# Optimization experiments

Measured on AMD Instinct MI355X. Metric: run time of the kernel, lower is better.

Reference implementation:

```python
import jax, jax.numpy as jnp
import numpy as np

ADMP = 8  # admp_channel -> K = ADMP*ADMP keypoints


def setup_inputs() -> dict:
    key = jax.random.key(0)
    kA, kB = jax.random.split(key)
    B, C, H, W = 8, 512, 96, 96
    feature_A = jax.random.normal(kA, (B, C, H, W), dtype=jnp.float32)
    feature_B = jax.random.normal(kB, (B, C, H, W), dtype=jnp.float32)
    return {"feature_A": feature_A, "feature_B": feature_B}


def _keypoint_rowcol(feature_A):
    # featureSelect: sum over channels, AdaptiveMaxPool2d(ADMP) with return_indices.
    # H,W divisible by ADMP so adaptive pool == uniform non-overlapping pooling.
    B, C, H, W = feature_A.shape
    ph, pw = H // ADMP, W // ADMP
    resp = feature_A.sum(axis=1)  # [B,H,W]
    r = resp.reshape(B, ADMP, ph, ADMP, pw).transpose(0, 1, 3, 2, 4)
    r = r.reshape(B, ADMP * ADMP, ph * pw)
    loc = jnp.argmax(r, axis=-1)  # first-max, matches torch  [B,K]
    kk = jnp.arange(ADMP * ADMP)
    gi, gj = kk // ADMP, kk % ADMP
    row_A = gi[None, :] * ph + loc // pw  # [B,K]
    col_A = gj[None, :] * pw + loc % pw
    return row_A, col_A


def reference(feature_A, feature_B):
    B, C, H, W = feature_A.shape
    K = ADMP * ADMP
    row_A, col_A = _keypoint_rowcol(feature_A)
    flat_A = row_A * W + col_A  # [B,K]

    # gather descriptors: [B,K,C]
    fa = feature_A.reshape(B, C, H * W)
    desc = jnp.take_along_axis(fa, flat_A[:, None, :], axis=2).transpose(0, 2, 1)

    # squared L2 distance map via ||b||^2 - 2 a.b + ||a||^2 : [B,K,HW]
    fb = feature_B.reshape(B, C, H * W)
    fb_sq = jnp.sum(fb * fb, axis=1)            # [B,HW]
    d_sq = jnp.sum(desc * desc, axis=-1)        # [B,K]
    cross = jnp.einsum('bkc,bcn->bkn', desc, fb)  # [B,K,HW]
    dist = fb_sq[:, None, :] - 2.0 * cross + d_sq[:, :, None]

    min_idx = jnp.argmin(dist, axis=-1)  # [B,K]
    row_B = min_idx // W
    col_B = min_idx % W
    drow = -(row_B - row_A)
    dcol = -(col_B - col_A)
    off = jnp.stack([drow, dcol], axis=-1)  # [B,K,2] int

    # getTranslationalOffsetByMode: most frequent (drow,dcol) pair per batch
    eq = jnp.all(off[:, :, None, :] == off[:, None, :, :], axis=-1)  # [B,K,K]
    counts = eq.sum(axis=-1)  # [B,K]
    best = jnp.argmax(counts, axis=-1)  # first occurrence on ties, matches dict order
    out = jnp.take_along_axis(off, best[:, None, None], axis=1)[:, 0, :]  # [B,2]
    return out
```

## Files before the change

kernel.cpp:

```cpp
#include <hip/hip_runtime.h>
#include <hip/hip_bf16.h>
#include <math.h>

typedef _Float16 half8 __attribute__((ext_vector_type(8)));
typedef __fp16 fp16x2 __attribute__((ext_vector_type(2)));
typedef float f32x4 __attribute__((ext_vector_type(4)));
typedef unsigned short u16x4 __attribute__((ext_vector_type(4)));
typedef unsigned short u16x8 __attribute__((ext_vector_type(8)));

#define B_   8
#define C_   512
#define H_   96
#define W_   96
#define HW   9216
#define K_   64
#define PH   12
#define PW   12
#define NT   96
#define CCH  32
#define NBLK 96

#define OFF_PARTIAL 0u
#define OFF_CANDV   0u
#define OFF_CANDN   294912u
#define OFF_DESCH   2359296u
#define OFF_DESCL   2883584u
#define OFF_ROWA    3407872u
#define OFF_COLA    3409920u

#define FBT_HI 0
#define FBT_LO 3072
#define DSC_HI 6144
#define DSC_LO 8704
#define BUFHW  11264

__global__ __launch_bounds__(256) void k_partial(const float* __restrict__ A,
                                                 float* __restrict__ part) {
    int idx4 = blockIdx.x * 256 + threadIdx.x;
    int chunk = blockIdx.y;
    int b = idx4 / (HW / 4), hw4 = idx4 - b * (HW / 4);
    const float* p = A + ((size_t)(b * C_ + chunk * 64)) * HW + hw4 * 4;
    float4 s = make_float4(0.f, 0.f, 0.f, 0.f);
#pragma unroll
    for (int i = 0; i < 64; ++i) {
        float4 v = *(const float4*)&p[(size_t)i * HW];
        s.x += v.x; s.y += v.y; s.z += v.z; s.w += v.w;
    }
    *(float4*)&part[chunk * (B_ * HW) + b * HW + hw4 * 4] = s;
}

__global__ void k_selgather(const float* __restrict__ part, const float* __restrict__ A,
                            int* __restrict__ rowA, int* __restrict__ colA,
                            _Float16* __restrict__ descH, _Float16* __restrict__ descL) {
    int k = blockIdx.x, b = blockIdx.y, lane = threadIdx.x;
    int gi = k >> 3, gj = k & 7;
    float bv = -1e30f; int bp = 1 << 20;
    for (int p = lane; p < PH * PW; p += 64) {
        int lr = p / PW, lc = p - lr * PW;
        int hw = (gi * PH + lr) * W_ + gj * PW + lc;
        float v = 0.f;
#pragma unroll
        for (int ch = 0; ch < 8; ++ch) v += part[ch * (B_ * HW) + b * HW + hw];
        if (v > bv || (v == bv && p < bp)) { bv = v; bp = p; }
    }
    for (int m = 1; m < 64; m <<= 1) {
        float ov = __shfl_xor(bv, m);
        int   op = __shfl_xor(bp, m);
        if (ov > bv || (ov == bv && op < bp)) { bv = ov; bp = op; }
    }
    int lr = bp / PW, lc = bp - lr * PW;
    int r = gi * PH + lr, c = gj * PW + lc;
    int flat = r * W_ + c;
    if (lane == 0) { rowA[b * K_ + k] = r; colA[b * K_ + k] = c; }
#pragma unroll
    for (int i = 0; i < 8; ++i) {
        int cc = i * 64 + lane;
        float v = A[((size_t)(b * C_ + cc)) * HW + flat];
        _Float16 h = (_Float16)v;
        _Float16 lo = (_Float16)((v - (float)h) * 2048.f);
        size_t o = ((size_t)(b * K_ + k)) * C_ + cc;
        descH[o] = h; descL[o] = lo;
    }
}

__global__ __launch_bounds__(256, 3) void k_main(const float* __restrict__ FB,
                                                 const _Float16* __restrict__ descH,
                                                 const _Float16* __restrict__ descL,
                                                 float* __restrict__ candV,
                                                 int* __restrict__ candN) {
    __shared__ __attribute__((aligned(16))) unsigned short smem_us[2 * BUFHW];
    int b = blockIdx.y, nb = blockIdx.x * NT;
    int tid = threadIdx.x;
    int l = tid & 63;
    int w = tid >> 6;
    const size_t baseB = (size_t)b * C_ * HW + nb;

    const int so = tid % 12;
    const int scb = tid / 12;
    const int st_nt = so >> 1, st_nn0 = (so & 1) * 8;
    const int dk = tid >> 2, dco = tid & 3;

    f32x4 accH[6], accX[6];
#pragma unroll
    for (int nt = 0; nt < 6; ++nt) {
        accH[nt] = (f32x4){0.f, 0.f, 0.f, 0.f};
        accX[nt] = (f32x4){0.f, 0.f, 0.f, 0.f};
    }
    float sq[8];
#pragma unroll
    for (int j = 0; j < 8; ++j) sq[j] = 0.f;

    float4 Ar0a, Ar0b, Ar1a, Ar1b; u16x8 ArdH, ArdL;
    float4 Br0a, Br0b, Br1a, Br1b; u16x8 BrdH, BrdL;

#define LOADALL(S, c0)                                                        \
    do {                                                                      \
        if (tid < 192) {                                                      \
            const float* p0 = &FB[baseB + (size_t)((c0) + scb) * HW + so * 8];      \
            const float* p1 = &FB[baseB + (size_t)((c0) + scb + 16) * HW + so * 8]; \
            S##r0a = *(const float4*)p0; S##r0b = *(const float4*)(p0 + 4);   \
            S##r1a = *(const float4*)p1; S##r1b = *(const float4*)(p1 + 4);   \
        }                                                                     \
        size_t o = ((size_t)(b * K_) + dk) * C_ + (c0) + dco * 8;             \
        S##rdH = *(const u16x8*)&descH[o];                                    \
        S##rdL = *(const u16x8*)&descL[o];                                    \
    } while (0)

#define CVT8(va, vb, hofs)                                                    \
    do {                                                                      \
        union { fp16x2 p[4]; half8 h; } hh, ll;                               \
        float vv[8] = {va.x, va.y, va.z, va.w, vb.x, vb.y, vb.z, vb.w};       \
        _Pragma("unroll")                                                     \
        for (int j = 0; j < 4; ++j) {                                         \
            float a = vv[2 * j], bq = vv[2 * j + 1];                          \
            fp16x2 hp = __builtin_amdgcn_cvt_pkrtz(a, bq);                    \
            float ha = (float)hp[0], hb = (float)hp[1];                       \
            fp16x2 lp = __builtin_amdgcn_cvt_pkrtz((a - ha) * 2048.f,         \
                                                   (bq - hb) * 2048.f);       \
            hh.p[j] = hp; ll.p[j] = lp;                                       \
            sq[2 * j]     = fmaf(a, a, sq[2 * j]);                            \
            sq[2 * j + 1] = fmaf(bq, bq, sq[2 * j + 1]);                      \
        }                                                                     \
        *(half8*)&smem_us[(hofs)] = hh.h;                                     \
        *(half8*)&smem_us[(hofs) + FBT_LO] = ll.h;                            \
    } while (0)

#define WRITEALL(S, bufhw)                                                    \
    do {                                                                      \
        if (tid < 192) {                                                      \
            int c = scb;                                                      \
            int off0 = (bufhw) + FBT_HI + st_nt * 512 + ((c >> 2) & 1) * 256  \
                       + (c >> 3) * 64 + (c & 3) * 16 + st_nn0;               \
            CVT8(S##r0a, S##r0b, off0);                                       \
            c = scb + 16;                                                     \
            int off1 = (bufhw) + FBT_HI + st_nt * 512 + ((c >> 2) & 1) * 256  \
                       + (c >> 3) * 64 + (c & 3) * 16 + st_nn0;               \
            CVT8(S##r1a, S##r1b, off1);                                       \
        }                                                                     \
        *(u16x8*)&smem_us[(bufhw) + DSC_HI + dk * 40 + dco * 8] = S##rdH;     \
        *(u16x8*)&smem_us[(bufhw) + DSC_LO + dk * 40 + dco * 8] = S##rdL;     \
    } while (0)

    const unsigned lds0 = (unsigned)(size_t)&smem_us[0];

#define TRQ(d0, d1, d2, d3, addr)                                             \
    asm volatile("ds_read_b64_tr_b16 %0, %1"             : "=v"(d0) : "v"(addr)); \
    asm volatile("ds_read_b64_tr_b16 %0, %1 offset:512"  : "=v"(d1) : "v"(addr)); \
    asm volatile("ds_read_b64_tr_b16 %0, %1 offset:6144" : "=v"(d2) : "v"(addr)); \
    asm volatile("ds_read_b64_tr_b16 %0, %1 offset:6656" : "=v"(d3) : "v"(addr));

#define WAIT8 asm volatile("s_waitcnt lgkmcnt(8)" ::: "memory");              \
              __builtin_amdgcn_sched_barrier(0);
#define WAIT4 asm volatile("s_waitcnt lgkmcnt(4)" ::: "memory");              \
              __builtin_amdgcn_sched_barrier(0);
#define WAIT0 asm volatile("s_waitcnt lgkmcnt(0)" ::: "memory");              \
              __builtin_amdgcn_sched_barrier(0);

#define MFMA3(nt, h0_, h1_, l0_, l1_)                                         \
    do {                                                                      \
        union { u16x4 q[2]; half8 h; } bh, bl;                                \
        bh.q[0] = h0_; bh.q[1] = h1_; bl.q[0] = l0_; bl.q[1] = l1_;           \
        accH[nt] = __builtin_amdgcn_mfma_f32_16x16x32_f16(aHu.h, bh.h, accH[nt], 0, 0, 0); \
        accX[nt] = __builtin_amdgcn_mfma_f32_16x16x32_f16(aHu.h, bl.h, accX[nt], 0, 0, 0); \
        accX[nt] = __builtin_amdgcn_mfma_f32_16x16x32_f16(aLu.h, bh.h, accX[nt], 0, 0, 0); \
    } while (0)

#define COMPUTE(cur)                                                          \
    do {                                                                      \
        union { u16x8 u; half8 h; } aHu, aLu;                                 \
        const unsigned abase = lds0 +                                         \
            (unsigned)((cur) + DSC_HI + (w * 16 + (l & 15)) * 40 + (l >> 4) * 8) * 2u; \
        __builtin_amdgcn_s_setprio(1);                                        \
        asm volatile("ds_read_b128 %0, %1"             : "=v"(aHu.u) : "v"(abase)); \
        asm volatile("ds_read_b128 %0, %1 offset:5120" : "=v"(aLu.u) : "v"(abase)); \
        const unsigned trb = lds0 + (unsigned)(cur) * 2u + (unsigned)l * 8u;  \
        u16x4 xh0, xh1, xl0, xl1, yh0, yh1, yl0, yl1, zh0, zh1, zl0, zl1;     \
        TRQ(xh0, xh1, xl0, xl1, trb);                                 \
        TRQ(yh0, yh1, yl0, yl1, trb + 1024u);                         \
        TRQ(zh0, zh1, zl0, zl1, trb + 2048u);                         \
        WAIT8;                                              \
        MFMA3(0, xh0, xh1, xl0, xl1);                                         \
        TRQ(xh0, xh1, xl0, xl1, trb + 3072u);                         \
        WAIT8;                                                  \
        MFMA3(1, yh0, yh1, yl0, yl1);                                         \
        TRQ(yh0, yh1, yl0, yl1, trb + 4096u);                         \
        WAIT8;                                                  \
        MFMA3(2, zh0, zh1, zl0, zl1);                                         \
        TRQ(zh0, zh1, zl0, zl1, trb + 5120u);                         \
        WAIT8;                                                  \
        MFMA3(3, xh0, xh1, xl0, xl1);                                         \
        WAIT4;                                                  \
        MFMA3(4, yh0, yh1, yl0, yl1);                                         \
        WAIT0;                                                  \
        MFMA3(5, zh0, zh1, zl0, zl1);                                         \
        __builtin_amdgcn_s_setprio(0);                                        \
    } while (0)

    LOADALL(A, 0);
    WRITEALL(A, 0);
    LOADALL(B, CCH);
    __syncthreads();

#pragma unroll 1
    for (int tp = 0; tp < 8; ++tp) {
        const int t0 = 2 * tp, t1 = 2 * tp + 1;
        if (t0 + 2 < 16) LOADALL(A, (t0 + 2) * CCH);
        COMPUTE(0);
        if (t0 + 1 < 16) WRITEALL(B, BUFHW);
        __syncthreads();
        if (t1 + 2 < 16) LOADALL(B, (t1 + 2) * CCH);
        COMPUTE(BUFHW);
        if (t1 + 1 < 16) WRITEALL(A, 0);
        __syncthreads();
    }

    float* fscr = (float*)&smem_us[0];
    if (tid < 192) {
        *(float4*)&fscr[scb * 96 + so * 8]     = make_float4(sq[0], sq[1], sq[2], sq[3]);
        *(float4*)&fscr[scb * 96 + so * 8 + 4] = make_float4(sq[4], sq[5], sq[6], sq[7]);
    }
    __syncthreads();
    if (tid < 96) {
        float s = 0.f;
#pragma unroll
        for (int g = 0; g < 16; ++g) s += fscr[g * 96 + tid];
        fscr[1536 + tid] = s;
    }
    __syncthreads();

    const float inv2048 = 1.f / 2048.f;
#pragma unroll
    for (int r = 0; r < 4; ++r) {
        float bv = 1e30f; int bn = 1 << 28;
#pragma unroll
        for (int nt = 0; nt < 6; ++nt) {
            float cross = accH[nt][r] + accX[nt][r] * inv2048;
            float d = fscr[1536 + nt * 16 + (l & 15)] - 2.f * cross;
            int n = nb + nt * 16 + (l & 15);
            if (d < bv) { bv = d; bn = n; }
        }
#pragma unroll
        for (int m = 1; m < 16; m <<= 1) {
            float ov = __shfl_xor(bv, m);
            int   on = __shfl_xor(bn, m);
            if (ov < bv || (ov == bv && on < bn)) { bv = ov; bn = on; }
        }
        if ((l & 15) == 0) {
            int k = w * 16 + (l >> 4) * 4 + r;
            candV[(b * K_ + k) * NBLK + blockIdx.x] = bv;
            candN[(b * K_ + k) * NBLK + blockIdx.x] = bn;
        }
    }
#undef LOADALL
#undef CVT8
#undef WRITEALL
#undef TRQ
#undef WAIT8
#undef WAIT4
#undef WAIT0
#undef MFMA3
#undef COMPUTE
}

__global__ void k_redmode(const float* __restrict__ candV, const int* __restrict__ candN,
                          const int* __restrict__ rowA, const int* __restrict__ colA,
                          int* __restrict__ out) {
    __shared__ int r_s[64], c_s[64];
    int b = blockIdx.x, k = threadIdx.x;
    int base = (b * K_ + k) * NBLK;
    float bv = 1e30f; int bn = 1 << 28;
    for (int j = 0; j < NBLK; ++j) {
        float ov = candV[base + j]; int on = candN[base + j];
        if (ov < bv || (ov == bv && on < bn)) { bv = ov; bn = on; }
    }
    int rB = bn / W_, cB = bn - rB * W_;
    r_s[k] = rowA[b * K_ + k] - rB;
    c_s[k] = colA[b * K_ + k] - cB;
    __syncthreads();
    int mr = r_s[k], mc = c_s[k], cnt = 0;
#pragma unroll
    for (int j = 0; j < 64; ++j) cnt += (r_s[j] == mr && c_s[j] == mc) ? 1 : 0;
    int bk = k, bc = cnt;
    for (int m = 1; m < 64; m <<= 1) {
        int oc = __shfl_xor(bc, m);
        int ok = __shfl_xor(bk, m);
        if (oc > bc || (oc == bc && ok < bk)) { bc = oc; bk = ok; }
    }
    if (k == 0) { out[b * 2] = r_s[bk]; out[b * 2 + 1] = c_s[bk]; }
}

extern "C" void kernel_launch(void* const* d_in, const int* in_sizes, int n_in,
                              void* d_out, int out_size, void* d_ws, size_t ws_size,
                              hipStream_t stream) {
    const float* A  = (const float*)d_in[0];
    const float* FB = (const float*)d_in[1];
    char* ws = (char*)d_ws;
    float*     part  = (float*)(ws + OFF_PARTIAL);
    _Float16*  descH = (_Float16*)(ws + OFF_DESCH);
    _Float16*  descL = (_Float16*)(ws + OFF_DESCL);
    int*       rowA  = (int*)(ws + OFF_ROWA);
    int*       colA  = (int*)(ws + OFF_COLA);
    float*     candV = (float*)(ws + OFF_CANDV);
    int*       candN = (int*)(ws + OFF_CANDN);
    int*       out   = (int*)d_out;

    k_partial<<<dim3((B_ * HW) / 1024, 8), 256, 0, stream>>>(A, part);
    k_selgather<<<dim3(K_, B_), 64, 0, stream>>>(part, A, rowA, colA, descH, descL);
    k_main<<<dim3(NBLK, B_), 256, 0, stream>>>(FB, descH, descL, candV, candN);
    k_redmode<<<dim3(B_), 64, 0, stream>>>(candV, candN, rowA, colA, out);
}
```

Baseline: 93.28 us.

## Replace per-block candidate arrays with packed 64-bit atomicMin and swizzle block order

k_main now packs each (distance, index) candidate into an order-preserving 64-bit key and reduces it with a global atomicMin into one slot per keypoint. This removes the candidate arrays and the serial 96-entry scan in k_redmode. The slots are reset to all-ones inside k_partial. Block indices in k_partial and k_main are also remapped (swizzled), which may change how blocks spread across XCDs and caches. The cost is atomic contention on 512 slots, and tie-breaking now relies on the packed-key ordering.

```diff
diff --git a/kernel.cpp b/kernel.cpp
--- a/kernel.cpp
+++ b/kernel.cpp
@@ -7,6 +7,7 @@
 typedef float f32x4 __attribute__((ext_vector_type(4)));
 typedef unsigned short u16x4 __attribute__((ext_vector_type(4)));
 typedef unsigned short u16x8 __attribute__((ext_vector_type(8)));
+typedef unsigned long long u64;
 
 #define B_   8
 #define C_   512
@@ -21,12 +22,11 @@
 #define NBLK 96
 
 #define OFF_PARTIAL 0u
-#define OFF_CANDV   0u
-#define OFF_CANDN   294912u
 #define OFF_DESCH   2359296u
 #define OFF_DESCL   2883584u
 #define OFF_ROWA    3407872u
 #define OFF_COLA    3409920u
+#define OFF_SLOTS   3411968u
 
 #define FBT_HI 0
 #define FBT_LO 3072
@@ -35,8 +35,14 @@
 #define BUFHW  11264
 
 __global__ __launch_bounds__(256) void k_partial(const float* __restrict__ A,
-                                                 float* __restrict__ part) {
-    int idx4 = blockIdx.x * 256 + threadIdx.x;
+                                                 float* __restrict__ part,
+                                                 u64* __restrict__ slots) {
+    if (blockIdx.x == 0 && blockIdx.y == 0) {
+        slots[threadIdx.x] = ~0ull;
+        slots[threadIdx.x + 256] = ~0ull;
+    }
+    int bxs = (blockIdx.x & 7) * 9 + (blockIdx.x >> 3);
+    int idx4 = bxs * 256 + threadIdx.x;
     int chunk = blockIdx.y;
     int b = idx4 / (HW / 4), hw4 = idx4 - b * (HW / 4);
     const float* p = A + ((size_t)(b * C_ + chunk * 64)) * HW + hw4 * 4;
@@ -86,10 +92,11 @@
 __global__ __launch_bounds__(256, 3) void k_main(const float* __restrict__ FB,
                                                  const _Float16* __restrict__ descH,
                                                  const _Float16* __restrict__ descL,
-                                                 float* __restrict__ candV,
-                                                 int* __restrict__ candN) {
+                                                 u64* __restrict__ slots) {
     __shared__ __attribute__((aligned(16))) unsigned short smem_us[2 * BUFHW];
-    int b = blockIdx.y, nb = blockIdx.x * NT;
+    int b = blockIdx.y;
+    int bxs = (blockIdx.x & 7) * 12 + (blockIdx.x >> 3);
+    int nb = bxs * NT;
     int tid = threadIdx.x;
     int l = tid & 63;
     int w = tid >> 6;
@@ -195,23 +202,23 @@
         asm volatile("ds_read_b128 %0, %1 offset:5120" : "=v"(aLu.u) : "v"(abase)); \
         const unsigned trb = lds0 + (unsigned)(cur) * 2u + (unsigned)l * 8u;  \
         u16x4 xh0, xh1, xl0, xl1, yh0, yh1, yl0, yl1, zh0, zh1, zl0, zl1;     \
-        TRQ(xh0, xh1, xl0, xl1, trb);                                 \
-        TRQ(yh0, yh1, yl0, yl1, trb + 1024u);                         \
-        TRQ(zh0, zh1, zl0, zl1, trb + 2048u);                         \
-        WAIT8;                                              \
+        TRQ(xh0, xh1, xl0, xl1, trb);                                         \
+        TRQ(yh0, yh1, yl0, yl1, trb + 1024u);                                 \
+        TRQ(zh0, zh1, zl0, zl1, trb + 2048u);                                 \
+        WAIT8;                                                                \
         MFMA3(0, xh0, xh1, xl0, xl1);                                         \
-        TRQ(xh0, xh1, xl0, xl1, trb + 3072u);                         \
-        WAIT8;                                                  \
+        TRQ(xh0, xh1, xl0, xl1, trb + 3072u);                                 \
+        WAIT8;                                                                \
         MFMA3(1, yh0, yh1, yl0, yl1);                                         \
-        TRQ(yh0, yh1, yl0, yl1, trb + 4096u);                         \
-        WAIT8;                                                  \
+        TRQ(yh0, yh1, yl0, yl1, trb + 4096u);                                 \
+        WAIT8;                                                                \
         MFMA3(2, zh0, zh1, zl0, zl1);                                         \
-        TRQ(zh0, zh1, zl0, zl1, trb + 5120u);                         \
-        WAIT8;                                                  \
+        TRQ(zh0, zh1, zl0, zl1, trb + 5120u);                                 \
+        WAIT8;                                                                \
         MFMA3(3, xh0, xh1, xl0, xl1);                                         \
-        WAIT4;                                                  \
+        WAIT4;                                                                \
         MFMA3(4, yh0, yh1, yl0, yl1);                                         \
-        WAIT0;                                                  \
+        WAIT0;                                                                \
         MFMA3(5, zh0, zh1, zl0, zl1);                                         \
         __builtin_amdgcn_s_setprio(0);                                        \
     } while (0)
@@ -267,8 +274,10 @@
         }
         if ((l & 15) == 0) {
             int k = w * 16 + (l >> 4) * 4 + r;
-            candV[(b * K_ + k) * NBLK + blockIdx.x] = bv;
-            candN[(b * K_ + k) * NBLK + blockIdx.x] = bn;
+            unsigned bits = __float_as_uint(bv);
+            unsigned key = (bits & 0x80000000u) ? ~bits : (bits | 0x80000000u);
+            u64 packed = ((u64)key << 32) | (unsigned)bn;
+            atomicMin(&slots[b * K_ + k], packed);
         }
     }
 #undef LOADALL
@@ -282,17 +291,13 @@
 #undef COMPUTE
 }
 
-__global__ void k_redmode(const float* __restrict__ candV, const int* __restrict__ candN,
+__global__ void k_redmode(const u64* __restrict__ slots,
                           const int* __restrict__ rowA, const int* __restrict__ colA,
                           int* __restrict__ out) {
     __shared__ int r_s[64], c_s[64];
     int b = blockIdx.x, k = threadIdx.x;
-    int base = (b * K_ + k) * NBLK;
-    float bv = 1e30f; int bn = 1 << 28;
-    for (int j = 0; j < NBLK; ++j) {
-        float ov = candV[base + j]; int on = candN[base + j];
-        if (ov < bv || (ov == bv && on < bn)) { bv = ov; bn = on; }
-    }
+    u64 s = slots[b * K_ + k];
+    int bn = (int)(unsigned)(s & 0xFFFFFFFFull);
     int rB = bn / W_, cB = bn - rB * W_;
     r_s[k] = rowA[b * K_ + k] - rB;
     c_s[k] = colA[b * K_ + k] - cB;
@@ -320,12 +325,11 @@
     _Float16*  descL = (_Float16*)(ws + OFF_DESCL);
     int*       rowA  = (int*)(ws + OFF_ROWA);
     int*       colA  = (int*)(ws + OFF_COLA);
-    float*     candV = (float*)(ws + OFF_CANDV);
-    int*       candN = (int*)(ws + OFF_CANDN);
+    u64*       slots = (u64*)(ws + OFF_SLOTS);
     int*       out   = (int*)d_out;
 
-    k_partial<<<dim3((B_ * HW) / 1024, 8), 256, 0, stream>>>(A, part);
+    k_partial<<<dim3((B_ * HW) / 1024, 8), 256, 0, stream>>>(A, part, slots);
     k_selgather<<<dim3(K_, B_), 64, 0, stream>>>(part, A, rowA, colA, descH, descL);
-    k_main<<<dim3(NBLK, B_), 256, 0, stream>>>(FB, descH, descL, candV, candN);
-    k_redmode<<<dim3(B_), 64, 0, stream>>>(candV, candN, rowA, colA, out);
-}
+    k_main<<<dim3(NBLK, B_), 256, 0, stream>>>(FB, descH, descL, slots);
+    k_redmode<<<dim3(B_), 64, 0, stream>>>(slots, rowA, colA, out);
+}
```

New measurement: 82.77 us. 1.13x faster.
